# Optimization experiments

Measured on AMD Instinct MI355X. Metric: run time of the kernel, lower is better.

The kernel has to match this reference:

```python
import jax, jax.numpy as jnp
import numpy as np

N_NODES = 100000
N_EDGES = 3200000
D_IN = 256
D_OUT = 256


def setup_inputs() -> dict:
    key = jax.random.key(0)
    k1, k2, k3, k4, k5 = jax.random.split(key, 5)
    x = jax.random.normal(k1, (N_NODES, D_IN), dtype=jnp.float32)
    weight = jax.random.normal(k2, (D_IN, D_OUT), dtype=jnp.float32) * (1.0 / np.sqrt(D_IN))
    edge_row = jax.random.randint(k3, (N_EDGES,), 0, N_NODES, dtype=jnp.int32)
    edge_col = jax.random.randint(k4, (N_EDGES,), 0, N_NODES, dtype=jnp.int32)
    edge_val = jax.random.uniform(k5, (N_EDGES,), dtype=jnp.float32)
    return {"x": x, "weight": weight, "edge_row": edge_row,
            "edge_col": edge_col, "edge_val": edge_val}


def reference(x, weight, edge_row, edge_col, edge_val):
    # support = dropout(x) @ W  (dropout p=0 -> identity, eval-mode math)
    support = x @ weight                       # [N, D_OUT]
    # output = spmm(adj, support): for each edge (r, c, v): out[r] += v * support[c]
    gathered = edge_val[:, None] * support[edge_col]   # [E, D_OUT]
    output = jax.ops.segment_sum(gathered, edge_row, num_segments=N_NODES)
    return output
```

## Files before the change

kernel.cpp:

```cpp
#include <hip/hip_runtime.h>

#define N_NODES 100000
#define N_EDGES 3200000
#define DIM 256

typedef _Float16 half_t;
typedef __attribute__((ext_vector_type(4))) _Float16 half4;
typedef __attribute__((ext_vector_type(8))) _Float16 half8;
typedef __attribute__((ext_vector_type(4))) float floatx4;

#define BM 128
#define BK 32
#define LDK 40
#define GEMM_BLOCKS 782

#define NBUCK 500
#define RPB 200
#define CAPG 8192
#define STRIDE_I2 25600
#define EPB 16384
#define NEB 196

__global__ __launch_bounds__(256) void castw_kernel(const float* __restrict__ w,
                                                    half_t* __restrict__ wT) {
    __shared__ float tile[32][33];
    int bk = blockIdx.x * 32;
    int bn = blockIdx.y * 32;
    int tx = threadIdx.x & 31, ty = threadIdx.x >> 5;
#pragma unroll
    for (int i = 0; i < 4; i++)
        tile[ty + i * 8][tx] = w[(size_t)(bk + ty + i * 8) * DIM + bn + tx];
    __syncthreads();
#pragma unroll
    for (int i = 0; i < 4; i++)
        wT[(size_t)(bn + ty + i * 8) * DIM + bk + tx] = (half_t)tile[tx][ty + i * 8];
}

__global__ __launch_bounds__(512) void gemm_scatter_kernel(
        const float* __restrict__ A, const half_t* __restrict__ BT,
        half_t* __restrict__ C,
        const int* __restrict__ erow, const int* __restrict__ ecol,
        const float* __restrict__ eval, int* __restrict__ bcursor,
        int2* __restrict__ tmp) {
    __shared__ __align__(16) char smem[30720];
    const int tid = threadIdx.x;

    if (blockIdx.x < GEMM_BLOCKS) {
        half_t (*As)[LDK] = (half_t (*)[LDK])smem;
        half_t (*Bs)[LDK] = (half_t (*)[LDK])(smem + 10240);

        const int wid = tid >> 6, lane = tid & 63;
        const int wm = wid & 1, wn = wid >> 1;
        const int row0 = blockIdx.x * BM;
        const int lr = lane & 15;
        const int quad = lane >> 4;

        floatx4 acc[4][4] = {};

        const int ar = tid >> 2;
        const int ac = (tid & 3) * 8;
        const bool avalid = (row0 + ar) < N_NODES;
        const float* aptr = A + (size_t)(row0 + ar) * DIM + ac;

        for (int k0 = 0; k0 < DIM; k0 += BK) {
            {
                const float4* src = (const float4*)(aptr + k0);
                half_t* dst = &As[ar][ac];
#pragma unroll
                for (int i = 0; i < 2; i++) {
                    float4 v = avalid ? src[i] : make_float4(0.f, 0.f, 0.f, 0.f);
                    half4 h;
                    h.x = (half_t)v.x; h.y = (half_t)v.y;
                    h.z = (half_t)v.z; h.w = (half_t)v.w;
                    ((half4*)dst)[i] = h;
                }
            }
            {
#pragma unroll
                for (int i = 0; i < 2; i++) {
                    int ch = tid + i * 512;
                    int r = ch >> 2, cb = (ch & 3) * 8;
                    half8 v = *(const half8*)(BT + (size_t)r * DIM + k0 + cb);
                    *(half8*)&Bs[r][cb] = v;
                }
            }
            __syncthreads();

            half8 a[4], b[4];
#pragma unroll
            for (int i = 0; i < 4; i++)
                a[i] = *(const half8*)&As[wm * 64 + i * 16 + lr][quad * 8];
#pragma unroll
            for (int j = 0; j < 4; j++)
                b[j] = *(const half8*)&Bs[wn * 64 + j * 16 + lr][quad * 8];
#pragma unroll
            for (int i = 0; i < 4; i++)
#pragma unroll
                for (int j = 0; j < 4; j++)
                    acc[i][j] = __builtin_amdgcn_mfma_f32_16x16x32_f16(
                        a[i], b[j], acc[i][j], 0, 0, 0);
            __syncthreads();
        }

#pragma unroll
        for (int i = 0; i < 4; i++) {
#pragma unroll
            for (int j = 0; j < 4; j++) {
                int gc = wn * 64 + j * 16 + lr;
                int grb = row0 + wm * 64 + i * 16 + quad * 4;
#pragma unroll
                for (int r = 0; r < 4; r++) {
                    int gr = grb + r;
                    if (gr < N_NODES) C[(size_t)gr * DIM + gc] = (half_t)acc[i][j][r];
                }
            }
        }
    } else {
        int* lh = (int*)smem;
        int* lbase = lh + NBUCK;
        const int sb = blockIdx.x - GEMM_BLOCKS;

        for (int b = tid; b < NBUCK; b += 512) lh[b] = 0;
        __syncthreads();

        int base4 = sb * (EPB / 4);
#pragma unroll
        for (int i = 0; i < 8; i++) {
            int idx4 = base4 + i * 512 + tid;
            if (idx4 < N_EDGES / 4) {
                int4 r4 = ((const int4*)erow)[idx4];
                atomicAdd(&lh[(unsigned)r4.x / RPB], 1);
                atomicAdd(&lh[(unsigned)r4.y / RPB], 1);
                atomicAdd(&lh[(unsigned)r4.z / RPB], 1);
                atomicAdd(&lh[(unsigned)r4.w / RPB], 1);
            }
        }
        __syncthreads();
        for (int b = tid; b < NBUCK; b += 512) {
            int c = lh[b];
            int st = 0;
            if (c) {
                st = atomicAdd(&bcursor[b * 16], c);
                if (st > CAPG - c) st = CAPG - c;
                if (st < 0) st = 0;
            }
            lbase[b] = b * STRIDE_I2 + st;
            lh[b] = 0;
        }
        __syncthreads();

#define SCAT(R, C, V)                                                      \
        {                                                                  \
            unsigned _r = (unsigned)(R); int _c = (C);                     \
            int _b = _r / RPB;                                             \
            int _rl = _r - _b * RPB;                                       \
            int _rank = atomicAdd(&lh[_b], 1);                             \
            tmp[lbase[_b] + _rank] =                                       \
                make_int2((_rl << 17) | _c, __float_as_int(V));            \
        }
#pragma unroll
        for (int i = 0; i < 8; i++) {
            int idx4 = base4 + i * 512 + tid;
            if (idx4 < N_EDGES / 4) {
                int4 r4 = ((const int4*)erow)[idx4];
                int4 c4 = ((const int4*)ecol)[idx4];
                float4 v4 = ((const float4*)eval)[idx4];
                SCAT(r4.x, c4.x, v4.x);
                SCAT(r4.y, c4.y, v4.y);
                SCAT(r4.z, c4.z, v4.z);
                SCAT(r4.w, c4.w, v4.w);
            }
        }
#undef SCAT
    }
}

__global__ __launch_bounds__(512, 4) void csr_spmm_kernel(
        const half_t* __restrict__ support, const int* __restrict__ bcnt,
        const int2* __restrict__ tmp, float* __restrict__ out) {
    __shared__ int lh[256];
    __shared__ int s[256];
    __shared__ int roff[257];
    __shared__ __align__(16) int2 ledge[CAPG];

    const int b = blockIdx.x;
    const int t = threadIdx.x;
    int cnt = bcnt[b * 16];
    if (cnt > CAPG) cnt = CAPG;
    const int2* src = tmp + (size_t)b * STRIDE_I2;
    const int row0 = b * RPB;

    if (t < 256) lh[t] = 0;
    __syncthreads();
    for (int e = t; e < cnt; e += 512)
        atomicAdd(&lh[src[e].x >> 17], 1);
    __syncthreads();

    if (t < 256) s[t] = lh[t];
    __syncthreads();
    for (int off = 1; off < 256; off <<= 1) {
        int u = 0;
        if (t < 256 && t >= off) u = s[t - off];
        __syncthreads();
        if (t < 256) s[t] += u;
        __syncthreads();
    }
    if (t < 256) {
        int ex = s[t] - lh[t];
        roff[t] = ex;
        lh[t] = ex;
    }
    if (t == 0) roff[256] = cnt;
    __syncthreads();

    for (int e = t; e < cnt; e += 512) {
        int2 q = src[e];
        int lr = q.x >> 17;
        int rank = atomicAdd(&lh[lr], 1);
        ledge[rank] = make_int2(q.x & 0x1FFFF, q.y);
    }
    __syncthreads();

    const int wid = t >> 6, lane = t & 63;
    const int h = lane >> 5;
    const int j = lane & 31;

    for (int r = wid; r < RPB; r += 8) {
        int row = row0 + r;
        int beg = roff[r];
        int end = roff[r + 1];

        float acc[8] = {0.f, 0.f, 0.f, 0.f, 0.f, 0.f, 0.f, 0.f};
        int e = beg;

        if ((e & 1) && e < end) {
            int2 q = ledge[e];
            half8 sv = *(const half8*)(support + (size_t)q.x * DIM + j * 8);
            float v = (h == 0) ? __int_as_float(q.y) : 0.f;
#pragma unroll
            for (int d = 0; d < 8; d++) acc[d] += v * (float)sv[d];
            e++;
        }

        for (; e + 15 < end; e += 16) {
            int4 pa = *(const int4*)&ledge[e + 2 * h];
            int4 pb = *(const int4*)&ledge[e + 4 + 2 * h];
            int4 pc = *(const int4*)&ledge[e + 8 + 2 * h];
            int4 pd = *(const int4*)&ledge[e + 12 + 2 * h];
            half8 s0 = *(const half8*)(support + (size_t)pa.x * DIM + j * 8);
            half8 s1 = *(const half8*)(support + (size_t)pa.z * DIM + j * 8);
            half8 s2 = *(const half8*)(support + (size_t)pb.x * DIM + j * 8);
            half8 s3 = *(const half8*)(support + (size_t)pb.z * DIM + j * 8);
            half8 s4 = *(const half8*)(support + (size_t)pc.x * DIM + j * 8);
            half8 s5 = *(const half8*)(support + (size_t)pc.z * DIM + j * 8);
            half8 s6 = *(const half8*)(support + (size_t)pd.x * DIM + j * 8);
            half8 s7 = *(const half8*)(support + (size_t)pd.z * DIM + j * 8);
            float v0 = __int_as_float(pa.y), v1 = __int_as_float(pa.w);
            float v2 = __int_as_float(pb.y), v3 = __int_as_float(pb.w);
            float v4 = __int_as_float(pc.y), v5 = __int_as_float(pc.w);
            float v6 = __int_as_float(pd.y), v7 = __int_as_float(pd.w);
#pragma unroll
            for (int d = 0; d < 8; d++)
                acc[d] += v0 * (float)s0[d] + v1 * (float)s1[d]
                        + v2 * (float)s2[d] + v3 * (float)s3[d]
                        + v4 * (float)s4[d] + v5 * (float)s5[d]
                        + v6 * (float)s6[d] + v7 * (float)s7[d];
        }
        for (; e + 1 < end; e += 2) {
            int2 q = ledge[e + h];
            half8 sv = *(const half8*)(support + (size_t)q.x * DIM + j * 8);
            float v = __int_as_float(q.y);
#pragma unroll
            for (int d = 0; d < 8; d++) acc[d] += v * (float)sv[d];
        }
        if (e < end) {
            int2 q = ledge[e];
            half8 sv = *(const half8*)(support + (size_t)q.x * DIM + j * 8);
            float v = (h == 0) ? __int_as_float(q.y) : 0.f;
#pragma unroll
            for (int d = 0; d < 8; d++) acc[d] += v * (float)sv[d];
        }

        float r0, r1, r2, r3, g0, g1, g2, g3;
        if (h == 0) {
            r0 = acc[0]; r1 = acc[1]; r2 = acc[2]; r3 = acc[3];
            g0 = acc[4]; g1 = acc[5]; g2 = acc[6]; g3 = acc[7];
        } else {
            r0 = acc[4]; r1 = acc[5]; r2 = acc[6]; r3 = acc[7];
            g0 = acc[0]; g1 = acc[1]; g2 = acc[2]; g3 = acc[3];
        }
        r0 += __shfl_xor(g0, 32, 64);
        r1 += __shfl_xor(g1, 32, 64);
        r2 += __shfl_xor(g2, 32, 64);
        r3 += __shfl_xor(g3, 32, 64);

        *(float4*)(out + (size_t)row * DIM + j * 8 + h * 4) =
            make_float4(r0, r1, r2, r3);
    }
}

extern "C" void kernel_launch(void* const* d_in, const int* in_sizes, int n_in,
                              void* d_out, int out_size, void* d_ws, size_t ws_size,
                              hipStream_t stream) {
    const float* x    = (const float*)d_in[0];
    const float* w    = (const float*)d_in[1];
    const int*   erow = (const int*)d_in[2];
    const int*   ecol = (const int*)d_in[3];
    const float* eval = (const float*)d_in[4];
    float* out = (float*)d_out;

    char* ws = (char*)d_ws;
    half_t* support = (half_t*)ws;
    half_t* wT      = (half_t*)(ws + 51200000);
    int*    bcnt    = (int*)(ws + 51331072);
    int2*   tmp     = (int2*)d_out;

    hipMemsetAsync(bcnt, 0, NBUCK * 16 * sizeof(int), stream);

    castw_kernel<<<dim3(8, 8), 256, 0, stream>>>(w, wT);

    gemm_scatter_kernel<<<GEMM_BLOCKS + NEB, 512, 0, stream>>>(
        x, wT, support, erow, ecol, eval, bcnt, tmp);

    csr_spmm_kernel<<<NBUCK, 512, 0, stream>>>(support, bcnt, tmp, out);
}
```

Baseline: 566.8 us.

## Split fused GEMM/scatter into separate histogram, scan, and staged compact scatter kernels

Separates the fused GEMM+edge-bucketing kernel into a standalone GEMM followed by a global histogram, an exclusive bucket scan, and a scatter kernel. The scatter kernel sorts edges locally in shared memory before writing them out in contiguous runs. Buckets now cover 128 rows, chosen with shifts instead of division, and the edge list is stored compactly by prefix offsets instead of in fixed-stride slots. This is meant to make scatter writes coalesced and smaller buckets raise SpMM occupancy. In exchange it adds extra launches, reads the row array a third time, and loses the overlap between GEMM and bucketing.

Measured after the change: 806.3 us. 1.42x slower.

```diff
diff --git a/kernel.cpp b/kernel.cpp
--- a/kernel.cpp
+++ b/kernel.cpp
@@ -12,14 +12,12 @@
 #define BM 128
 #define BK 32
 #define LDK 40
-#define GEMM_BLOCKS 782
-
-#define NBUCK 500
-#define RPB 200
-#define CAPG 8192
-#define STRIDE_I2 25600
-#define EPB 16384
-#define NEB 196
+
+#define NBUCK 782
+#define RPB 128
+#define CAPG 4608
+#define EPB 8192
+#define NEB 391
 
 __global__ __launch_bounds__(256) void castw_kernel(const float* __restrict__ w,
                                                     half_t* __restrict__ wT) {
@@ -36,181 +34,254 @@
         wT[(size_t)(bn + ty + i * 8) * DIM + bk + tx] = (half_t)tile[tx][ty + i * 8];
 }
 
-__global__ __launch_bounds__(512) void gemm_scatter_kernel(
-        const float* __restrict__ A, const half_t* __restrict__ BT,
-        half_t* __restrict__ C,
-        const int* __restrict__ erow, const int* __restrict__ ecol,
-        const float* __restrict__ eval, int* __restrict__ bcursor,
-        int2* __restrict__ tmp) {
-    __shared__ __align__(16) char smem[30720];
+__global__ __launch_bounds__(512) void gemm_f16_kernel(const float* __restrict__ A,
+                                                       const half_t* __restrict__ BT,
+                                                       half_t* __restrict__ C, int M) {
+    __shared__ half_t As[BM][LDK];
+    __shared__ half_t Bs[256][LDK];
+
     const int tid = threadIdx.x;
-
-    if (blockIdx.x < GEMM_BLOCKS) {
-        half_t (*As)[LDK] = (half_t (*)[LDK])smem;
-        half_t (*Bs)[LDK] = (half_t (*)[LDK])(smem + 10240);
-
-        const int wid = tid >> 6, lane = tid & 63;
-        const int wm = wid & 1, wn = wid >> 1;
-        const int row0 = blockIdx.x * BM;
-        const int lr = lane & 15;
-        const int quad = lane >> 4;
-
-        floatx4 acc[4][4] = {};
-
-        const int ar = tid >> 2;
-        const int ac = (tid & 3) * 8;
-        const bool avalid = (row0 + ar) < N_NODES;
-        const float* aptr = A + (size_t)(row0 + ar) * DIM + ac;
-
-        for (int k0 = 0; k0 < DIM; k0 += BK) {
-            {
-                const float4* src = (const float4*)(aptr + k0);
-                half_t* dst = &As[ar][ac];
-#pragma unroll
-                for (int i = 0; i < 2; i++) {
-                    float4 v = avalid ? src[i] : make_float4(0.f, 0.f, 0.f, 0.f);
-                    half4 h;
-                    h.x = (half_t)v.x; h.y = (half_t)v.y;
-                    h.z = (half_t)v.z; h.w = (half_t)v.w;
-                    ((half4*)dst)[i] = h;
-                }
+    const int wid = tid >> 6, lane = tid & 63;
+    const int wm = wid & 1, wn = wid >> 1;
+    const int row0 = blockIdx.x * BM;
+    const int lr = lane & 15;
+    const int quad = lane >> 4;
+
+    floatx4 acc[4][4] = {};
+
+    const int ar = tid >> 2;
+    const int ac = (tid & 3) * 8;
+    const bool avalid = (row0 + ar) < M;
+    const float* aptr = A + (size_t)(row0 + ar) * DIM + ac;
+
+    for (int k0 = 0; k0 < DIM; k0 += BK) {
+        {
+            const float4* src = (const float4*)(aptr + k0);
+            half_t* dst = &As[ar][ac];
+#pragma unroll
+            for (int i = 0; i < 2; i++) {
+                float4 v = avalid ? src[i] : make_float4(0.f, 0.f, 0.f, 0.f);
+                half4 h;
+                h.x = (half_t)v.x; h.y = (half_t)v.y;
+                h.z = (half_t)v.z; h.w = (half_t)v.w;
+                ((half4*)dst)[i] = h;
             }
-            {
-#pragma unroll
-                for (int i = 0; i < 2; i++) {
-                    int ch = tid + i * 512;
-                    int r = ch >> 2, cb = (ch & 3) * 8;
-                    half8 v = *(const half8*)(BT + (size_t)r * DIM + k0 + cb);
-                    *(half8*)&Bs[r][cb] = v;
-                }
+        }
+        {
+#pragma unroll
+            for (int i = 0; i < 2; i++) {
+                int ch = tid + i * 512;
+                int r = ch >> 2, cb = (ch & 3) * 8;
+                half8 v = *(const half8*)(BT + (size_t)r * DIM + k0 + cb);
+                *(half8*)&Bs[r][cb] = v;
             }
-            __syncthreads();
-
-            half8 a[4], b[4];
-#pragma unroll
-            for (int i = 0; i < 4; i++)
-                a[i] = *(const half8*)&As[wm * 64 + i * 16 + lr][quad * 8];
+        }
+        __syncthreads();
+
+        half8 a[4], b[4];
+#pragma unroll
+        for (int i = 0; i < 4; i++)
+            a[i] = *(const half8*)&As[wm * 64 + i * 16 + lr][quad * 8];
+#pragma unroll
+        for (int j = 0; j < 4; j++)
+            b[j] = *(const half8*)&Bs[wn * 64 + j * 16 + lr][quad * 8];
+#pragma unroll
+        for (int i = 0; i < 4; i++)
 #pragma unroll
             for (int j = 0; j < 4; j++)
-                b[j] = *(const half8*)&Bs[wn * 64 + j * 16 + lr][quad * 8];
-#pragma unroll
-            for (int i = 0; i < 4; i++)
-#pragma unroll
-                for (int j = 0; j < 4; j++)
-                    acc[i][j] = __builtin_amdgcn_mfma_f32_16x16x32_f16(
-                        a[i], b[j], acc[i][j], 0, 0, 0);
-            __syncthreads();
-        }
-
-#pragma unroll
-        for (int i = 0; i < 4; i++) {
-#pragma unroll
-            for (int j = 0; j < 4; j++) {
-                int gc = wn * 64 + j * 16 + lr;
-                int grb = row0 + wm * 64 + i * 16 + quad * 4;
-#pragma unroll
-                for (int r = 0; r < 4; r++) {
-                    int gr = grb + r;
-                    if (gr < N_NODES) C[(size_t)gr * DIM + gc] = (half_t)acc[i][j][r];
-                }
+                acc[i][j] = __builtin_amdgcn_mfma_f32_16x16x32_f16(a[i], b[j], acc[i][j], 0, 0, 0);
+        __syncthreads();
+    }
+
+#pragma unroll
+    for (int i = 0; i < 4; i++) {
+#pragma unroll
+        for (int j = 0; j < 4; j++) {
+            int gc = wn * 64 + j * 16 + lr;
+            int grb = row0 + wm * 64 + i * 16 + quad * 4;
+#pragma unroll
+            for (int r = 0; r < 4; r++) {
+                int gr = grb + r;
+                if (gr < M) C[(size_t)gr * DIM + gc] = (half_t)acc[i][j][r];
             }
         }
-    } else {
-        int* lh = (int*)smem;
-        int* lbase = lh + NBUCK;
-        const int sb = blockIdx.x - GEMM_BLOCKS;
-
-        for (int b = tid; b < NBUCK; b += 512) lh[b] = 0;
-        __syncthreads();
-
-        int base4 = sb * (EPB / 4);
-#pragma unroll
-        for (int i = 0; i < 8; i++) {
-            int idx4 = base4 + i * 512 + tid;
-            if (idx4 < N_EDGES / 4) {
-                int4 r4 = ((const int4*)erow)[idx4];
-                atomicAdd(&lh[(unsigned)r4.x / RPB], 1);
-                atomicAdd(&lh[(unsigned)r4.y / RPB], 1);
-                atomicAdd(&lh[(unsigned)r4.z / RPB], 1);
-                atomicAdd(&lh[(unsigned)r4.w / RPB], 1);
-            }
-        }
-        __syncthreads();
-        for (int b = tid; b < NBUCK; b += 512) {
-            int c = lh[b];
-            int st = 0;
-            if (c) {
-                st = atomicAdd(&bcursor[b * 16], c);
-                if (st > CAPG - c) st = CAPG - c;
-                if (st < 0) st = 0;
-            }
-            lbase[b] = b * STRIDE_I2 + st;
-            lh[b] = 0;
-        }
-        __syncthreads();
+    }
+}
+
+__global__ __launch_bounds__(512) void hist_kernel(const int* __restrict__ erow,
+                                                   int* __restrict__ bcnt) {
+    __shared__ int lh[NBUCK];
+    for (int b = threadIdx.x; b < NBUCK; b += 512) lh[b] = 0;
+    __syncthreads();
+    int base4 = blockIdx.x * (EPB / 4);
+#pragma unroll
+    for (int i = 0; i < 4; i++) {
+        int idx4 = base4 + i * 512 + threadIdx.x;
+        if (idx4 < N_EDGES / 4) {
+            int4 r4 = ((const int4*)erow)[idx4];
+            atomicAdd(&lh[r4.x >> 7], 1);
+            atomicAdd(&lh[r4.y >> 7], 1);
+            atomicAdd(&lh[r4.z >> 7], 1);
+            atomicAdd(&lh[r4.w >> 7], 1);
+        }
+    }
+    __syncthreads();
+    for (int b = threadIdx.x; b < NBUCK; b += 512)
+        if (lh[b]) atomicAdd(&bcnt[b * 16], lh[b]);
+}
+
+__global__ __launch_bounds__(512) void scan_buckets_kernel(int* __restrict__ bcnt,
+                                                           int* __restrict__ bbase) {
+    __shared__ int s[1024];
+    int t = threadIdx.x;
+    int v0 = (t < NBUCK) ? bcnt[t * 16] : 0;
+    int v1 = (t + 512 < NBUCK) ? bcnt[(t + 512) * 16] : 0;
+    s[t] = v0; s[t + 512] = v1;
+    __syncthreads();
+    for (int off = 1; off < 1024; off <<= 1) {
+        int a = (t >= off) ? s[t - off] : 0;
+        int b = (t + 512 >= off) ? s[t + 512 - off] : 0;
+        __syncthreads();
+        s[t] += a; s[t + 512] += b;
+        __syncthreads();
+    }
+    if (t < NBUCK) {
+        int ex = s[t] - v0;
+        bbase[t] = ex;
+        bcnt[t * 16] = ex;
+    }
+    if (t + 512 < NBUCK) {
+        int ex = s[t + 512] - v1;
+        bbase[t + 512] = ex;
+        bcnt[(t + 512) * 16] = ex;
+    }
+    if (t == 0) bbase[NBUCK] = N_EDGES;
+}
+
+__global__ __launch_bounds__(512, 4) void scatter_kernel(const int* __restrict__ erow,
+                                                         const int* __restrict__ ecol,
+                                                         const float* __restrict__ eval,
+                                                         int* __restrict__ gcur,
+                                                         int2* __restrict__ tmp) {
+    __shared__ int lh[NBUCK];
+    __shared__ int lstart[NBUCK + 1];
+    __shared__ int gbase[NBUCK];
+    __shared__ int ssum[1024];
+    __shared__ __align__(16) int2 stage[EPB];
+
+    const int t = threadIdx.x;
+    for (int b = t; b < NBUCK; b += 512) lh[b] = 0;
+    __syncthreads();
+
+    int base4 = blockIdx.x * (EPB / 4);
+#pragma unroll
+    for (int i = 0; i < 4; i++) {
+        int idx4 = base4 + i * 512 + t;
+        if (idx4 < N_EDGES / 4) {
+            int4 r4 = ((const int4*)erow)[idx4];
+            atomicAdd(&lh[r4.x >> 7], 1);
+            atomicAdd(&lh[r4.y >> 7], 1);
+            atomicAdd(&lh[r4.z >> 7], 1);
+            atomicAdd(&lh[r4.w >> 7], 1);
+        }
+    }
+    __syncthreads();
+    int v0 = (t < NBUCK) ? lh[t] : 0;
+    int v1 = (t + 512 < NBUCK) ? lh[t + 512] : 0;
+    ssum[t] = v0; ssum[t + 512] = v1;
+    __syncthreads();
+    for (int off = 1; off < 1024; off <<= 1) {
+        int a = (t >= off) ? ssum[t - off] : 0;
+        int b = (t + 512 >= off) ? ssum[t + 512 - off] : 0;
+        __syncthreads();
+        ssum[t] += a; ssum[t + 512] += b;
+        __syncthreads();
+    }
+    if (t < NBUCK) {
+        int ex = ssum[t] - v0;
+        lstart[t] = ex;
+        gbase[t] = v0 ? atomicAdd(&gcur[t * 16], v0) : 0;
+        lh[t] = ex;
+    }
+    if (t + 512 < NBUCK) {
+        int ex = ssum[t + 512] - v1;
+        lstart[t + 512] = ex;
+        gbase[t + 512] = v1 ? atomicAdd(&gcur[(t + 512) * 16], v1) : 0;
+        lh[t + 512] = ex;
+    }
+    if (t == NBUCK - 512) lstart[NBUCK] = ssum[NBUCK - 1];
+    __syncthreads();
 
 #define SCAT(R, C, V)                                                      \
-        {                                                                  \
-            unsigned _r = (unsigned)(R); int _c = (C);                     \
-            int _b = _r / RPB;                                             \
-            int _rl = _r - _b * RPB;                                       \
-            int _rank = atomicAdd(&lh[_b], 1);                             \
-            tmp[lbase[_b] + _rank] =                                       \
-                make_int2((_rl << 17) | _c, __float_as_int(V));            \
-        }
-#pragma unroll
-        for (int i = 0; i < 8; i++) {
-            int idx4 = base4 + i * 512 + tid;
-            if (idx4 < N_EDGES / 4) {
-                int4 r4 = ((const int4*)erow)[idx4];
-                int4 c4 = ((const int4*)ecol)[idx4];
-                float4 v4 = ((const float4*)eval)[idx4];
-                SCAT(r4.x, c4.x, v4.x);
-                SCAT(r4.y, c4.y, v4.y);
-                SCAT(r4.z, c4.z, v4.z);
-                SCAT(r4.w, c4.w, v4.w);
-            }
-        }
+    {                                                                      \
+        int _r = (R), _c = (C);                                            \
+        int _b = _r >> 7;                                                  \
+        int _rank = atomicAdd(&lh[_b], 1);                                 \
+        stage[_rank] = make_int2(((_r & 127) << 17) | _c, __float_as_int(V)); \
+    }
+#pragma unroll
+    for (int i = 0; i < 4; i++) {
+        int idx4 = base4 + i * 512 + t;
+        if (idx4 < N_EDGES / 4) {
+            int4 r4 = ((const int4*)erow)[idx4];
+            int4 c4 = ((const int4*)ecol)[idx4];
+            float4 v4 = ((const float4*)eval)[idx4];
+            SCAT(r4.x, c4.x, v4.x);
+            SCAT(r4.y, c4.y, v4.y);
+            SCAT(r4.z, c4.z, v4.z);
+            SCAT(r4.w, c4.w, v4.w);
+        }
+    }
 #undef SCAT
-    }
-}
-
-__global__ __launch_bounds__(512, 4) void csr_spmm_kernel(
-        const half_t* __restrict__ support, const int* __restrict__ bcnt,
+    __syncthreads();
+
+    const int wid = t >> 6, lane = t & 63;
+    for (int b = wid; b < NBUCK; b += 8) {
+        int ls = lstart[b];
+        int n = lstart[b + 1] - ls;
+        int gb = gbase[b];
+        for (int c = lane; c < n; c += 64)
+            tmp[(size_t)gb + c] = stage[ls + c];
+    }
+}
+
+__global__ __launch_bounds__(512, 8) void csr_spmm_kernel(
+        const half_t* __restrict__ support, const int* __restrict__ bbase,
         const int2* __restrict__ tmp, float* __restrict__ out) {
-    __shared__ int lh[256];
-    __shared__ int s[256];
-    __shared__ int roff[257];
+    __shared__ int lh[RPB];
+    __shared__ int s[RPB];
+    __shared__ int roff[RPB + 1];
     __shared__ __align__(16) int2 ledge[CAPG];
 
     const int b = blockIdx.x;
     const int t = threadIdx.x;
-    int cnt = bcnt[b * 16];
+    const int beg = bbase[b];
+    int cnt = bbase[b + 1] - beg;
     if (cnt > CAPG) cnt = CAPG;
-    const int2* src = tmp + (size_t)b * STRIDE_I2;
+    const int2* src = tmp + beg;
     const int row0 = b * RPB;
 
-    if (t < 256) lh[t] = 0;
+    if (t < RPB) lh[t] = 0;
     __syncthreads();
     for (int e = t; e < cnt; e += 512)
         atomicAdd(&lh[src[e].x >> 17], 1);
     __syncthreads();
 
-    if (t < 256) s[t] = lh[t];
-    __syncthreads();
-    for (int off = 1; off < 256; off <<= 1) {
+    if (t < RPB) s[t] = lh[t];
+    __syncthreads();
+    for (int off = 1; off < RPB; off <<= 1) {
         int u = 0;
-        if (t < 256 && t >= off) u = s[t - off];
-        __syncthreads();
-        if (t < 256) s[t] += u;
-        __syncthreads();
-    }
-    if (t < 256) {
+        if (t < RPB && t >= off) u = s[t - off];
+        __syncthreads();
+        if (t < RPB) s[t] += u;
+        __syncthreads();
+    }
+    if (t < RPB) {
         int ex = s[t] - lh[t];
         roff[t] = ex;
         lh[t] = ex;
     }
-    if (t == 0) roff[256] = cnt;
+    if (t == 0) roff[RPB] = cnt;
     __syncthreads();
 
     for (int e = t; e < cnt; e += 512) {
@@ -227,11 +298,11 @@
 
     for (int r = wid; r < RPB; r += 8) {
         int row = row0 + r;
-        int beg = roff[r];
+        if (row >= N_NODES) continue;
+        int e = roff[r];
         int end = roff[r + 1];
 
         float acc[8] = {0.f, 0.f, 0.f, 0.f, 0.f, 0.f, 0.f, 0.f};
-        int e = beg;
 
         if ((e & 1) && e < end) {
             int2 q = ledge[e];
@@ -313,14 +384,18 @@
     half_t* support = (half_t*)ws;
     half_t* wT      = (half_t*)(ws + 51200000);
     int*    bcnt    = (int*)(ws + 51331072);
-    int2*   tmp     = (int2*)d_out;
+    int*    bbase   = (int*)(ws + 51381120);
+    int2*   tmp     = (int2*)(ws + 51384256);
 
     hipMemsetAsync(bcnt, 0, NBUCK * 16 * sizeof(int), stream);
 
     castw_kernel<<<dim3(8, 8), 256, 0, stream>>>(w, wT);
 
-    gemm_scatter_kernel<<<GEMM_BLOCKS + NEB, 512, 0, stream>>>(
-        x, wT, support, erow, ecol, eval, bcnt, tmp);
-
-    csr_spmm_kernel<<<NBUCK, 512, 0, stream>>>(support, bcnt, tmp, out);
-}
+    dim3 ggrid((N_NODES + BM - 1) / BM, 1);
+    gemm_f16_kernel<<<ggrid, 512, 0, stream>>>(x, wT, support, N_NODES);
+
+    hist_kernel<<<NEB, 512, 0, stream>>>(erow, bcnt);
+    scan_buckets_kernel<<<1, 512, 0, stream>>>(bcnt, bbase);
+    scatter_kernel<<<NEB, 512, 0, stream>>>(erow, ecol, eval, bcnt, tmp);
+    csr_spmm_kernel<<<NBUCK, 512, 0, stream>>>(support, bbase, tmp, out);
+}
```
